# Kernel tuning notes

Measured on AMD Instinct MI355X. Metric: run time of the kernel, lower is better.

## Reference

```python
import jax, jax.numpy as jnp
import numpy as np

K = 10        # n_functions (random MLP draws)
H = 20        # hidden width of each tiny per-feature MLP
LN_EPS = 1e-5 # torch LayerNorm default eps
STD_EPS = 1e-8


def _layernorm(h):
    # LayerNorm over last dim, affine weight=1, bias=0 (torch default init),
    # biased variance, eps=1e-5.
    mu = h.mean(-1, keepdims=True)
    var = ((h - mu) ** 2).mean(-1, keepdims=True)
    return (h - mu) * jax.lax.rsqrt(var + LN_EPS)


def setup_inputs() -> dict:
    key = jax.random.key(0)
    B, T, N = 128, 256, 16
    ks = jax.random.split(key, 7)
    inputs = jax.random.normal(ks[0], (B, T, N), dtype=jnp.float32)

    def u(k, shape, bound):
        return jax.random.uniform(k, shape, minval=-bound, maxval=bound, dtype=jnp.float32)

    # torch Linear default init: uniform(-1/sqrt(fan_in), 1/sqrt(fan_in)) for W and b
    W1 = u(ks[1], (K, N, H), 1.0)        # Linear(1,20): fan_in=1
    b1 = u(ks[2], (K, N, H), 1.0)
    bnd = 1.0 / np.sqrt(H)
    W2 = u(ks[3], (K, N, H, H), bnd)     # Linear(20,20), weight layout [out,in]
    b2 = u(ks[4], (K, N, H), bnd)
    W3 = u(ks[5], (K, N, H), bnd)        # Linear(20,1) weight squeezed to [H]
    b3 = u(ks[6], (K, N), bnd)
    return {"inputs": inputs, "W1": W1, "b1": b1, "W2": W2, "b2": b2, "W3": W3, "b3": b3}


def reference(inputs, W1, b1, W2, b2, W3, b3):
    x = inputs.astype(jnp.float32)
    # standardize over batch dim (torch .std is unbiased, ddof=1)
    x = (x - x.mean(0)) / x.std(0, ddof=1)

    # All K draws x all N per-feature MLPs as one batched computation.
    # h: [K, B, T, N, H]
    h = jax.nn.relu(x[None, ..., None] * W1[:, None, None] + b1[:, None, None])
    h = _layernorm(h)
    h = jax.nn.relu(jnp.einsum('kbtni,knoi->kbtno', h, W2) + b2[:, None, None])
    h = _layernorm(h)
    t = jnp.einsum('kbtni,kni->kbtn', h, W3) + b3[:, None, None]   # [K, B, T, N]

    # std_out: standardize over batch dim
    t = (t - t.mean(1, keepdims=True)) / (t.std(1, ddof=1, keepdims=True) + STD_EPS)

    m_marginals = t.mean(1)                   # [K, T, N]
    prod_marginals = jnp.prod(m_marginals, -1)  # [K, T]
    prod_joint = jnp.prod(t, -1).mean(1)        # [K, T]
    per_k_mse = jnp.mean((prod_marginals - prod_joint) ** 2, axis=-1)  # [K]
    return jnp.mean(per_k_mse)
```

## Files before the change

### kernel.cpp

```cpp
#include <hip/hip_runtime.h>
#include <math.h>

#define B_ 128
#define T_ 256
#define N_ 16
#define K_ 10
#define H_ 20
#define TN_ (T_ * N_)
#define S_ (T_ * B_)

#define REP20(F) F(0) F(1) F(2) F(3) F(4) F(5) F(6) F(7) F(8) F(9) \
                 F(10) F(11) F(12) F(13) F(14) F(15) F(16) F(17) F(18) F(19)
#define REP16(F) F(0) F(1) F(2) F(3) F(4) F(5) F(6) F(7) F(8) F(9) \
                 F(10) F(11) F(12) F(13) F(14) F(15)

__device__ __forceinline__ float wsum(float v)
{
#pragma unroll
    for (int off = 32; off; off >>= 1) v += __shfl_xor(v, off);
    return v;
}

__global__ __launch_bounds__(256) void k_std(const float* __restrict__ x,
                                             float* __restrict__ xs2)
{
    const int wid = (blockIdx.x * 256 + threadIdx.x) >> 6;
    const int l   = threadIdx.x & 63;
    const int tt  = wid >> 4;
    const int n   = wid & 15;

    const float a0 = x[l * TN_ + wid];
    const float a1 = x[(64 + l) * TN_ + wid];

    const float sm = wsum(a0 + a1);
    const float mu = sm * (1.f / 128.f);

    const float d0 = a0 - mu, d1 = a1 - mu;
    const float vv = wsum(fmaf(d0, d0, d1 * d1));
    const float r  = __builtin_amdgcn_rsqf(vv * (1.f / 127.f));

    float* col = xs2 + ((size_t)n * T_ + tt) * B_;
    col[l]      = d0 * r;
    col[64 + l] = d1 * r;
}

__global__ __launch_bounds__(256) void k_mlp(
    const float* __restrict__ xs2,
    const float* __restrict__ W1, const float* __restrict__ b1,
    const float* __restrict__ W2, const float* __restrict__ b2,
    const float* __restrict__ W3, const float* __restrict__ b3,
    float* __restrict__ tb)
{
    const int kn = blockIdx.y;
    const int n  = kn & 15;

    const float* __restrict__ w1  = W1 + kn * H_;
    const float* __restrict__ bb1 = b1 + kn * H_;
    const float* __restrict__ w2  = W2 + kn * H_ * H_;
    const float* __restrict__ bb2 = b2 + kn * H_;
    const float* __restrict__ w3  = W3 + kn * H_;
    const float  bb3 = b3[kn];

    const int q = blockIdx.x * 256 + threadIdx.x;
    const float u = xs2[n * S_ + q];

#define DECLH(i) float h##i;
    REP20(DECLH)
    float s1 = 0.f;
#define L1(i) h##i = fmaxf(fmaf(u, w1[i], bb1[i]), 0.f); s1 += h##i;
    REP20(L1)
    const float mu1 = s1 * (1.f / H_);
    float v1 = 0.f;
#define VAR1(i) { const float d = h##i - mu1; v1 = fmaf(d, d, v1); }
    REP20(VAR1)
    const float r1  = __builtin_amdgcn_rsqf(v1 * (1.f / H_) + 1e-5f);
    const float mr1 = mu1 * r1;
#define NRM1(i) h##i = fmaf(h##i, r1, -mr1);
    REP20(NRM1)

#define DECLG(i) float g##i;
    REP20(DECLG)
    float s2 = 0.f;
#define L2I(o, i) acc = fmaf(h##i, w2[(o) * 20 + (i)], acc);
#define L2ROW(o) { float acc = bb2[o]; \
    L2I(o,0) L2I(o,1) L2I(o,2) L2I(o,3) L2I(o,4) \
    L2I(o,5) L2I(o,6) L2I(o,7) L2I(o,8) L2I(o,9) \
    L2I(o,10) L2I(o,11) L2I(o,12) L2I(o,13) L2I(o,14) \
    L2I(o,15) L2I(o,16) L2I(o,17) L2I(o,18) L2I(o,19) \
    g##o = fmaxf(acc, 0.f); s2 += g##o; }
    REP20(L2ROW)

    const float mu2 = s2 * (1.f / H_);
    float v2 = 0.f;
#define VAR2(o) { const float d = g##o - mu2; v2 = fmaf(d, d, v2); }
    REP20(VAR2)
    const float r2  = __builtin_amdgcn_rsqf(v2 * (1.f / H_) + 1e-5f);
    const float mr2 = mu2 * r2;

    float t = bb3;
#define L3(o) t = fmaf(fmaf(g##o, r2, -mr2), w3[o], t);
    REP20(L3)

    const int tt = q >> 7;
    const int b  = q & 127;
    tb[(((size_t)(kn >> 4) * T_ + tt) * N_ + n) * B_ + b] = t;
}

__global__ __launch_bounds__(256) void k_out(const float* __restrict__ tb,
                                             float* __restrict__ out)
{
    const int gw = (blockIdx.x * 256 + threadIdx.x) >> 6;
    const int l  = threadIdx.x & 63;
    const float* __restrict__ base = tb + (size_t)gw * (N_ * B_);

#define DECLZ(n) float z0_##n = base[(n) * B_ + l], z1_##n = base[(n) * B_ + 64 + l];
    REP16(DECLZ)

#define STDZ(n) { \
    const float sm = wsum(z0_##n + z1_##n); \
    const float mu = sm * (1.f / 128.f); \
    const float d0 = z0_##n - mu, d1 = z1_##n - mu; \
    const float vv = wsum(fmaf(d0, d0, d1 * d1)); \
    const float rr = 1.f / (sqrtf(vv * (1.f / 127.f)) + 1e-8f); \
    z0_##n = d0 * rr; z1_##n = d1 * rr; }
    REP16(STDZ)

    float p0 = 1.f, p1 = 1.f;
#define PRODZ(n) p0 *= z0_##n; p1 *= z1_##n;
    REP16(PRODZ)
    const float pj = wsum(p0 + p1) * (1.f / 128.f);

    if (l == 0)
        atomicAdd(out, pj * pj * (1.f / (K_ * T_)));
}

extern "C" void kernel_launch(void* const* d_in, const int* in_sizes, int n_in,
                              void* d_out, int out_size, void* d_ws, size_t ws_size,
                              hipStream_t stream)
{
    const float* x  = (const float*)d_in[0];
    const float* W1 = (const float*)d_in[1];
    const float* b1 = (const float*)d_in[2];
    const float* W2 = (const float*)d_in[3];
    const float* b2 = (const float*)d_in[4];
    const float* W3 = (const float*)d_in[5];
    const float* b3 = (const float*)d_in[6];
    float* out = (float*)d_out;

    char* ws = (char*)d_ws;
    float* xs2 = (float*)ws;
    float* tb  = (float*)(ws + (size_t)2 * 1024 * 1024);

    hipMemsetAsync(out, 0, sizeof(float), stream);

    k_std<<<(TN_ * 64) / 256, 256, 0, stream>>>(x, xs2);

    dim3 g2(S_ / 256, K_ * N_);
    k_mlp<<<g2, 256, 0, stream>>>(xs2, W1, b1, W2, b2, W3, b3, tb);

    k_out<<<(K_ * T_ * 64) / 256, 256, 0, stream>>>(tb, out);
}
```

Before: 199.4 us.

## Fuse standardization, per-feature MLP and output reduction into one kernel

Replaces the three-kernel pipeline with one kernel per (32 columns of T*N, k) block. The block stages inputs in shared memory, standardizes each column over the batch, runs the MLP with each lane handling two batch elements, standardizes outputs, and reduces the products in shared memory. This removes the global-memory round trips for the standardized inputs and the MLP outputs, plus two launches. In exchange, the batch standardization is recomputed for every k, the grid is only 1280 blocks, and register pressure is higher under a 3-waves-per-SIMD launch bound.

```diff
diff --git a/kernel.cpp b/kernel.cpp
--- a/kernel.cpp
+++ b/kernel.cpp
@@ -6,13 +6,11 @@
 #define N_ 16
 #define K_ 10
 #define H_ 20
-#define TN_ (T_ * N_)
-#define S_ (T_ * B_)
+#define TN_ 4096
+#define TQ_ 128
 
 #define REP20(F) F(0) F(1) F(2) F(3) F(4) F(5) F(6) F(7) F(8) F(9) \
                  F(10) F(11) F(12) F(13) F(14) F(15) F(16) F(17) F(18) F(19)
-#define REP16(F) F(0) F(1) F(2) F(3) F(4) F(5) F(6) F(7) F(8) F(9) \
-                 F(10) F(11) F(12) F(13) F(14) F(15)
 
 __device__ __forceinline__ float wsum(float v)
 {
@@ -21,117 +19,144 @@
     return v;
 }
 
-__global__ __launch_bounds__(256) void k_std(const float* __restrict__ x,
-                                             float* __restrict__ xs2)
-{
-    const int wid = (blockIdx.x * 256 + threadIdx.x) >> 6;
-    const int l   = threadIdx.x & 63;
-    const int tt  = wid >> 4;
-    const int n   = wid & 15;
-
-    const float a0 = x[l * TN_ + wid];
-    const float a1 = x[(64 + l) * TN_ + wid];
-
-    const float sm = wsum(a0 + a1);
-    const float mu = sm * (1.f / 128.f);
-
-    const float d0 = a0 - mu, d1 = a1 - mu;
-    const float vv = wsum(fmaf(d0, d0, d1 * d1));
-    const float r  = __builtin_amdgcn_rsqf(vv * (1.f / 127.f));
-
-    float* col = xs2 + ((size_t)n * T_ + tt) * B_;
-    col[l]      = d0 * r;
-    col[64 + l] = d1 * r;
-}
-
-__global__ __launch_bounds__(256) void k_mlp(
-    const float* __restrict__ xs2,
+__global__ __launch_bounds__(256, 3) void k_all(
+    const float* __restrict__ x,
     const float* __restrict__ W1, const float* __restrict__ b1,
     const float* __restrict__ W2, const float* __restrict__ b2,
     const float* __restrict__ W3, const float* __restrict__ b3,
-    float* __restrict__ tb)
+    float* __restrict__ out)
 {
-    const int kn = blockIdx.y;
-    const int n  = kn & 15;
+    __shared__ float xz[32 * 129];
+    __shared__ float zl[32 * 128];
+    __shared__ float pjp[4];
 
-    const float* __restrict__ w1  = W1 + kn * H_;
-    const float* __restrict__ bb1 = b1 + kn * H_;
-    const float* __restrict__ w2  = W2 + kn * H_ * H_;
-    const float* __restrict__ bb2 = b2 + kn * H_;
-    const float* __restrict__ w3  = W3 + kn * H_;
-    const float  bb3 = b3[kn];
+    const int tq  = blockIdx.x;
+    const int k   = blockIdx.y;
+    const int tid = threadIdx.x;
+    const int wv  = tid >> 6;
+    const int l   = tid & 63;
 
-    const int q = blockIdx.x * 256 + threadIdx.x;
-    const float u = xs2[n * S_ + q];
+#pragma unroll
+    for (int r = 0; r < 4; ++r) {
+        const int g4 = r * 1024 + tid * 4;
+        const int b  = g4 >> 5;
+        const int d0 = g4 & 31;
+        const float4 v = *reinterpret_cast<const float4*>(x + b * TN_ + tq * 32 + d0);
+        xz[(d0 + 0) * 129 + b] = v.x;
+        xz[(d0 + 1) * 129 + b] = v.y;
+        xz[(d0 + 2) * 129 + b] = v.z;
+        xz[(d0 + 3) * 129 + b] = v.w;
+    }
+    __syncthreads();
 
-#define DECLH(i) float h##i;
-    REP20(DECLH)
-    float s1 = 0.f;
-#define L1(i) h##i = fmaxf(fmaf(u, w1[i], bb1[i]), 0.f); s1 += h##i;
-    REP20(L1)
-    const float mu1 = s1 * (1.f / H_);
-    float v1 = 0.f;
-#define VAR1(i) { const float d = h##i - mu1; v1 = fmaf(d, d, v1); }
-    REP20(VAR1)
-    const float r1  = __builtin_amdgcn_rsqf(v1 * (1.f / H_) + 1e-5f);
-    const float mr1 = mu1 * r1;
-#define NRM1(i) h##i = fmaf(h##i, r1, -mr1);
-    REP20(NRM1)
+#pragma unroll
+    for (int c = 0; c < 8; ++c) {
+        const int col = wv * 8 + c;
+        const float a0 = xz[col * 129 + l];
+        const float a1 = xz[col * 129 + 64 + l];
+        const float mu = wsum(a0 + a1) * (1.f / 128.f);
+        const float d0 = a0 - mu, d1 = a1 - mu;
+        const float r  = __builtin_amdgcn_rsqf(wsum(fmaf(d0, d0, d1 * d1)) * (1.f / 127.f));
+        xz[col * 129 + l]      = d0 * r;
+        xz[col * 129 + 64 + l] = d1 * r;
+    }
+    __syncthreads();
 
-#define DECLG(i) float g##i;
-    REP20(DECLG)
-    float s2 = 0.f;
-#define L2I(o, i) acc = fmaf(h##i, w2[(o) * 20 + (i)], acc);
-#define L2ROW(o) { float acc = bb2[o]; \
-    L2I(o,0) L2I(o,1) L2I(o,2) L2I(o,3) L2I(o,4) \
-    L2I(o,5) L2I(o,6) L2I(o,7) L2I(o,8) L2I(o,9) \
-    L2I(o,10) L2I(o,11) L2I(o,12) L2I(o,13) L2I(o,14) \
-    L2I(o,15) L2I(o,16) L2I(o,17) L2I(o,18) L2I(o,19) \
-    g##o = fmaxf(acc, 0.f); s2 += g##o; }
-    REP20(L2ROW)
+#pragma unroll 1
+    for (int it = 0; it < 8; ++it) {
+        const int col = wv * 8 + it;
+        const int kn  = k * 16 + (col & 15);
 
-    const float mu2 = s2 * (1.f / H_);
-    float v2 = 0.f;
-#define VAR2(o) { const float d = g##o - mu2; v2 = fmaf(d, d, v2); }
-    REP20(VAR2)
-    const float r2  = __builtin_amdgcn_rsqf(v2 * (1.f / H_) + 1e-5f);
-    const float mr2 = mu2 * r2;
+        const float u0 = xz[col * 129 + l];
+        const float u1 = xz[col * 129 + 64 + l];
 
-    float t = bb3;
-#define L3(o) t = fmaf(fmaf(g##o, r2, -mr2), w3[o], t);
-    REP20(L3)
+        const float4* __restrict__ w1v = reinterpret_cast<const float4*>(W1 + kn * 20);
+        const float4* __restrict__ b1v = reinterpret_cast<const float4*>(b1 + kn * 20);
+        const float4* __restrict__ w2v = reinterpret_cast<const float4*>(W2 + kn * 400);
+        const float4* __restrict__ b2v = reinterpret_cast<const float4*>(b2 + kn * 20);
+        const float4* __restrict__ w3v = reinterpret_cast<const float4*>(W3 + kn * 20);
+        const float  bb3 = b3[kn];
 
-    const int tt = q >> 7;
-    const int b  = q & 127;
-    tb[(((size_t)(kn >> 4) * T_ + tt) * N_ + n) * B_ + b] = t;
-}
+#define DECLH(i) float ha##i, hb##i;
+        REP20(DECLH)
+        float s1a = 0.f, s1b = 0.f;
+#define L1C(c,i0,i1,i2,i3) { const float4 w = w1v[c]; const float4 bb = b1v[c]; \
+        ha##i0 = fmaxf(fmaf(u0, w.x, bb.x), 0.f); hb##i0 = fmaxf(fmaf(u1, w.x, bb.x), 0.f); s1a += ha##i0; s1b += hb##i0; \
+        ha##i1 = fmaxf(fmaf(u0, w.y, bb.y), 0.f); hb##i1 = fmaxf(fmaf(u1, w.y, bb.y), 0.f); s1a += ha##i1; s1b += hb##i1; \
+        ha##i2 = fmaxf(fmaf(u0, w.z, bb.z), 0.f); hb##i2 = fmaxf(fmaf(u1, w.z, bb.z), 0.f); s1a += ha##i2; s1b += hb##i2; \
+        ha##i3 = fmaxf(fmaf(u0, w.w, bb.w), 0.f); hb##i3 = fmaxf(fmaf(u1, w.w, bb.w), 0.f); s1a += ha##i3; s1b += hb##i3; }
+        L1C(0,0,1,2,3) L1C(1,4,5,6,7) L1C(2,8,9,10,11) L1C(3,12,13,14,15) L1C(4,16,17,18,19)
 
-__global__ __launch_bounds__(256) void k_out(const float* __restrict__ tb,
-                                             float* __restrict__ out)
-{
-    const int gw = (blockIdx.x * 256 + threadIdx.x) >> 6;
-    const int l  = threadIdx.x & 63;
-    const float* __restrict__ base = tb + (size_t)gw * (N_ * B_);
+        const float mu1a = s1a * 0.05f, mu1b = s1b * 0.05f;
+        float v1a = 0.f, v1b = 0.f;
+#define VAR1(i) { float d = ha##i - mu1a; v1a = fmaf(d, d, v1a); d = hb##i - mu1b; v1b = fmaf(d, d, v1b); }
+        REP20(VAR1)
+        const float r1a = __builtin_amdgcn_rsqf(v1a * 0.05f + 1e-5f);
+        const float r1b = __builtin_amdgcn_rsqf(v1b * 0.05f + 1e-5f);
+        const float m1a = mu1a * r1a, m1b = mu1b * r1b;
+#define NRM1(i) ha##i = fmaf(ha##i, r1a, -m1a); hb##i = fmaf(hb##i, r1b, -m1b);
+        REP20(NRM1)
 
-#define DECLZ(n) float z0_##n = base[(n) * B_ + l], z1_##n = base[(n) * B_ + 64 + l];
-    REP16(DECLZ)
+#define DECLG(i) float ga##i, gb##i;
+        REP20(DECLG)
+        float s2a = 0.f, s2b = 0.f;
+#define L2C(o,c,i0,i1,i2,i3) { const float4 w = w2v[(o) * 5 + (c)]; \
+        acca = fmaf(ha##i0, w.x, acca); acca = fmaf(ha##i1, w.y, acca); \
+        acca = fmaf(ha##i2, w.z, acca); acca = fmaf(ha##i3, w.w, acca); \
+        accb = fmaf(hb##i0, w.x, accb); accb = fmaf(hb##i1, w.y, accb); \
+        accb = fmaf(hb##i2, w.z, accb); accb = fmaf(hb##i3, w.w, accb); }
+#define L2ROW(o,bo) { float acca = (bo), accb = (bo); \
+        L2C(o,0,0,1,2,3) L2C(o,1,4,5,6,7) L2C(o,2,8,9,10,11) \
+        L2C(o,3,12,13,14,15) L2C(o,4,16,17,18,19) \
+        ga##o = fmaxf(acca, 0.f); s2a += ga##o; gb##o = fmaxf(accb, 0.f); s2b += gb##o; }
+        {
+            const float4 b2c0 = b2v[0], b2c1 = b2v[1], b2c2 = b2v[2], b2c3 = b2v[3], b2c4 = b2v[4];
+            L2ROW(0,  b2c0.x) L2ROW(1,  b2c0.y) L2ROW(2,  b2c0.z) L2ROW(3,  b2c0.w)
+            L2ROW(4,  b2c1.x) L2ROW(5,  b2c1.y) L2ROW(6,  b2c1.z) L2ROW(7,  b2c1.w)
+            L2ROW(8,  b2c2.x) L2ROW(9,  b2c2.y) L2ROW(10, b2c2.z) L2ROW(11, b2c2.w)
+            L2ROW(12, b2c3.x) L2ROW(13, b2c3.y) L2ROW(14, b2c3.z) L2ROW(15, b2c3.w)
+            L2ROW(16, b2c4.x) L2ROW(17, b2c4.y) L2ROW(18, b2c4.z) L2ROW(19, b2c4.w)
+        }
 
-#define STDZ(n) { \
-    const float sm = wsum(z0_##n + z1_##n); \
-    const float mu = sm * (1.f / 128.f); \
-    const float d0 = z0_##n - mu, d1 = z1_##n - mu; \
-    const float vv = wsum(fmaf(d0, d0, d1 * d1)); \
-    const float rr = 1.f / (sqrtf(vv * (1.f / 127.f)) + 1e-8f); \
-    z0_##n = d0 * rr; z1_##n = d1 * rr; }
-    REP16(STDZ)
+        const float mu2a = s2a * 0.05f, mu2b = s2b * 0.05f;
+        float v2a = 0.f, v2b = 0.f;
+#define VAR2(i) { float d = ga##i - mu2a; v2a = fmaf(d, d, v2a); d = gb##i - mu2b; v2b = fmaf(d, d, v2b); }
+        REP20(VAR2)
+        const float r2a = __builtin_amdgcn_rsqf(v2a * 0.05f + 1e-5f);
+        const float r2b = __builtin_amdgcn_rsqf(v2b * 0.05f + 1e-5f);
+        const float m2a = mu2a * r2a, m2b = mu2b * r2b;
 
-    float p0 = 1.f, p1 = 1.f;
-#define PRODZ(n) p0 *= z0_##n; p1 *= z1_##n;
-    REP16(PRODZ)
-    const float pj = wsum(p0 + p1) * (1.f / 128.f);
+        float t0 = bb3, t1 = bb3;
+#define L3C(c,i0,i1,i2,i3) { const float4 w = w3v[c]; \
+        t0 = fmaf(fmaf(ga##i0, r2a, -m2a), w.x, t0); t1 = fmaf(fmaf(gb##i0, r2b, -m2b), w.x, t1); \
+        t0 = fmaf(fmaf(ga##i1, r2a, -m2a), w.y, t0); t1 = fmaf(fmaf(gb##i1, r2b, -m2b), w.y, t1); \
+        t0 = fmaf(fmaf(ga##i2, r2a, -m2a), w.z, t0); t1 = fmaf(fmaf(gb##i2, r2b, -m2b), w.z, t1); \
+        t0 = fmaf(fmaf(ga##i3, r2a, -m2a), w.w, t0); t1 = fmaf(fmaf(gb##i3, r2b, -m2b), w.w, t1); }
+        L3C(0,0,1,2,3) L3C(1,4,5,6,7) L3C(2,8,9,10,11) L3C(3,12,13,14,15) L3C(4,16,17,18,19)
 
-    if (l == 0)
-        atomicAdd(out, pj * pj * (1.f / (K_ * T_)));
+        const float smu = wsum(t0 + t1) * (1.f / 128.f);
+        const float e0 = t0 - smu, e1 = t1 - smu;
+        const float sd = sqrtf(wsum(fmaf(e0, e0, e1 * e1)) * (1.f / 127.f));
+        const float rr = 1.f / (sd + 1e-8f);
+        zl[col * 128 + l]      = e0 * rr;
+        zl[col * 128 + 64 + l] = e1 * rr;
+    }
+    __syncthreads();
+
+    {
+        const int t_loc = wv >> 1;
+        const int b     = (wv & 1) * 64 + l;
+        float pj = zl[(t_loc * 16 + 0) * 128 + b];
+#pragma unroll
+        for (int n = 1; n < 16; ++n) pj *= zl[(t_loc * 16 + n) * 128 + b];
+        const float ps = wsum(pj);
+        if (l == 0) pjp[wv] = ps;
+    }
+    __syncthreads();
+    if (tid < 2) {
+        const float pjm = (pjp[tid * 2] + pjp[tid * 2 + 1]) * (1.f / 128.f);
+        atomicAdd(out, pjm * pjm * (1.f / (K_ * T_)));
+    }
 }
 
 extern "C" void kernel_launch(void* const* d_in, const int* in_sizes, int n_in,
@@ -147,16 +172,8 @@
     const float* b3 = (const float*)d_in[6];
     float* out = (float*)d_out;
 
-    char* ws = (char*)d_ws;
-    float* xs2 = (float*)ws;
-    float* tb  = (float*)(ws + (size_t)2 * 1024 * 1024);
-
     hipMemsetAsync(out, 0, sizeof(float), stream);
 
-    k_std<<<(TN_ * 64) / 256, 256, 0, stream>>>(x, xs2);
-
-    dim3 g2(S_ / 256, K_ * N_);
-    k_mlp<<<g2, 256, 0, stream>>>(xs2, W1, b1, W2, b2, W3, b3, tb);
-
-    k_out<<<(K_ * T_ * 64) / 256, 256, 0, stream>>>(tb, out);
+    dim3 grid(TQ_, K_);
+    k_all<<<grid, 256, 0, stream>>>(x, W1, b1, W2, b2, W3, b3, out);
 }
```

After: 236.4 us. 18.6% more time.

## Run hidden 20x20 layer on bf16 MFMA with hi/lo split and fused LN epilogue

Applied to the files above, without the earlier changes.

The per-thread scalar 20x20 FMA layer is replaced by MFMA 16x16x32 bf16 matrix ops. Activations and weights are staged in shared memory and split into hi/lo bf16 parts, using three MFMAs to approximate fp32 accuracy. The second LayerNorm and the W3 projection are folded into a one-pass sum/sumsq/dot reduction across lanes. The final atomicAdd is replaced by per-row partials plus a double-precision reduction kernel, and the memset is removed. This adds LDS traffic and shuffles, and drops the lo*lo term, which lowers precision slightly.

```diff
diff --git a/kernel.cpp b/kernel.cpp
--- a/kernel.cpp
+++ b/kernel.cpp
@@ -6,8 +6,13 @@
 #define N_ 16
 #define K_ 10
 #define H_ 20
-#define TN_ (T_ * N_)
-#define S_ (T_ * B_)
+#define TN_ 4096
+#define S_ 32768
+
+typedef __attribute__((ext_vector_type(8))) short bf16x8;
+typedef __attribute__((ext_vector_type(4))) float f32x4;
+
+union U4B { uint4 u; bf16x8 b; };
 
 #define REP20(F) F(0) F(1) F(2) F(3) F(4) F(5) F(6) F(7) F(8) F(9) \
                  F(10) F(11) F(12) F(13) F(14) F(15) F(16) F(17) F(18) F(19)
@@ -21,6 +26,15 @@
     return v;
 }
 
+__device__ __forceinline__ void split2(float a, float b, unsigned& hi, unsigned& lo)
+{
+    const unsigned au = __float_as_uint(a), bu = __float_as_uint(b);
+    hi = (au >> 16) | (bu & 0xffff0000u);
+    const float ra = a - __uint_as_float(au & 0xffff0000u);
+    const float rb = b - __uint_as_float(bu & 0xffff0000u);
+    lo = (__float_as_uint(ra) >> 16) | (__float_as_uint(rb) & 0xffff0000u);
+}
+
 __global__ __launch_bounds__(256) void k_std(const float* __restrict__ x,
                                              float* __restrict__ xs2)
 {
@@ -32,12 +46,9 @@
     const float a0 = x[l * TN_ + wid];
     const float a1 = x[(64 + l) * TN_ + wid];
 
-    const float sm = wsum(a0 + a1);
-    const float mu = sm * (1.f / 128.f);
-
+    const float mu = wsum(a0 + a1) * (1.f / 128.f);
     const float d0 = a0 - mu, d1 = a1 - mu;
-    const float vv = wsum(fmaf(d0, d0, d1 * d1));
-    const float r  = __builtin_amdgcn_rsqf(vv * (1.f / 127.f));
+    const float r  = __builtin_amdgcn_rsqf(wsum(fmaf(d0, d0, d1 * d1)) * (1.f / 127.f));
 
     float* col = xs2 + ((size_t)n * T_ + tt) * B_;
     col[l]      = d0 * r;
@@ -51,87 +62,177 @@
     const float* __restrict__ W3, const float* __restrict__ b3,
     float* __restrict__ tb)
 {
-    const int kn = blockIdx.y;
-    const int n  = kn & 15;
-
-    const float* __restrict__ w1  = W1 + kn * H_;
-    const float* __restrict__ bb1 = b1 + kn * H_;
-    const float* __restrict__ w2  = W2 + kn * H_ * H_;
-    const float* __restrict__ bb2 = b2 + kn * H_;
-    const float* __restrict__ w3  = W3 + kn * H_;
+    __shared__ unsigned hs[256 * 28];
+    __shared__ unsigned wB[32 * 28];
+    __shared__ float sb2[32], sw3[32];
+
+    const int kn  = blockIdx.y;
+    const int k   = kn >> 4;
+    const int n   = kn & 15;
+    const int tid = threadIdx.x;
+    const int w   = tid >> 6;
+    const int L   = tid & 63;
+    const int g   = L >> 4;
+    const int r16 = L & 15;
+    const int q0b = blockIdx.x * 256;
+
+    const float* __restrict__ w2c = W2 + kn * 400;
+    for (int j = tid; j < 320; j += 256) {
+        const int o = j / 10, kp = j % 10;
+        unsigned hi = 0u, lo = 0u;
+        if (o < 20)
+            split2(w2c[o * 20 + 2 * kp], w2c[o * 20 + 2 * kp + 1], hi, lo);
+        wB[o * 28 + kp]      = hi;
+        wB[o * 28 + 12 + kp] = lo;
+    }
+    if (tid < 128) {
+        const int o = tid >> 2, c = tid & 3;
+        wB[o * 28 + ((c < 2) ? 10 + c : 20 + c)] = 0u;
+    }
+    if (tid < 32) {
+        sb2[tid] = (tid < 20) ? b2[kn * 20 + tid] : 0.f;
+        sw3[tid] = (tid < 20) ? W3[kn * 20 + tid] : 0.f;
+    }
+
+    const float* __restrict__ w1c = W1 + kn * H_;
+    const float* __restrict__ b1c = b1 + kn * H_;
+    const float* __restrict__ w3c = W3 + kn * H_;
     const float  bb3 = b3[kn];
-
-    const int q = blockIdx.x * 256 + threadIdx.x;
-    const float u = xs2[n * S_ + q];
-
+    float w3sum = 0.f;
+#define W3S(i) w3sum += w3c[i];
+    REP20(W3S)
+
+    const float u = xs2[n * S_ + q0b + tid];
 #define DECLH(i) float h##i;
     REP20(DECLH)
     float s1 = 0.f;
-#define L1(i) h##i = fmaxf(fmaf(u, w1[i], bb1[i]), 0.f); s1 += h##i;
+#define L1(i) h##i = fmaxf(fmaf(u, w1c[i], b1c[i]), 0.f); s1 += h##i;
     REP20(L1)
-    const float mu1 = s1 * (1.f / H_);
+    const float mu1 = s1 * 0.05f;
     float v1 = 0.f;
 #define VAR1(i) { const float d = h##i - mu1; v1 = fmaf(d, d, v1); }
     REP20(VAR1)
-    const float r1  = __builtin_amdgcn_rsqf(v1 * (1.f / H_) + 1e-5f);
-    const float mr1 = mu1 * r1;
-#define NRM1(i) h##i = fmaf(h##i, r1, -mr1);
+    const float r1 = __builtin_amdgcn_rsqf(v1 * 0.05f + 1e-5f);
+    const float m1 = mu1 * r1;
+#define NRM1(i) h##i = fmaf(h##i, r1, -m1);
     REP20(NRM1)
 
-#define DECLG(i) float g##i;
-    REP20(DECLG)
-    float s2 = 0.f;
-#define L2I(o, i) acc = fmaf(h##i, w2[(o) * 20 + (i)], acc);
-#define L2ROW(o) { float acc = bb2[o]; \
-    L2I(o,0) L2I(o,1) L2I(o,2) L2I(o,3) L2I(o,4) \
-    L2I(o,5) L2I(o,6) L2I(o,7) L2I(o,8) L2I(o,9) \
-    L2I(o,10) L2I(o,11) L2I(o,12) L2I(o,13) L2I(o,14) \
-    L2I(o,15) L2I(o,16) L2I(o,17) L2I(o,18) L2I(o,19) \
-    g##o = fmaxf(acc, 0.f); s2 += g##o; }
-    REP20(L2ROW)
-
-    const float mu2 = s2 * (1.f / H_);
-    float v2 = 0.f;
-#define VAR2(o) { const float d = g##o - mu2; v2 = fmaf(d, d, v2); }
-    REP20(VAR2)
-    const float r2  = __builtin_amdgcn_rsqf(v2 * (1.f / H_) + 1e-5f);
-    const float mr2 = mu2 * r2;
-
-    float t = bb3;
-#define L3(o) t = fmaf(fmaf(g##o, r2, -mr2), w3[o], t);
-    REP20(L3)
-
-    const int tt = q >> 7;
-    const int b  = q & 127;
-    tb[(((size_t)(kn >> 4) * T_ + tt) * N_ + n) * B_ + b] = t;
-}
-
-__global__ __launch_bounds__(256) void k_out(const float* __restrict__ tb,
-                                             float* __restrict__ out)
-{
-    const int gw = (blockIdx.x * 256 + threadIdx.x) >> 6;
+    {
+        unsigned* row = hs + tid * 28;
+        unsigned hi, lo;
+#define PKW(m, i0, i1) split2(h##i0, h##i1, hi, lo); row[m] = hi; row[12 + m] = lo;
+        PKW(0, 0, 1) PKW(1, 2, 3) PKW(2, 4, 5) PKW(3, 6, 7) PKW(4, 8, 9)
+        PKW(5, 10, 11) PKW(6, 12, 13) PKW(7, 14, 15) PKW(8, 16, 17) PKW(9, 18, 19)
+        *reinterpret_cast<uint2*>(row + 10) = make_uint2(0u, 0u);
+        *reinterpret_cast<uint2*>(row + 22) = make_uint2(0u, 0u);
+    }
+    __syncthreads();
+
+    const int slhi = (g < 2) ? g * 4 : 8;
+    const int sllo = 12 + slhi;
+    U4B bh0, bl0, bh1, bl1;
+    bh0.u = *reinterpret_cast<const uint4*>(wB + r16 * 28 + slhi);
+    bl0.u = *reinterpret_cast<const uint4*>(wB + r16 * 28 + sllo);
+    bh1.u = *reinterpret_cast<const uint4*>(wB + (16 + r16) * 28 + slhi);
+    bl1.u = *reinterpret_cast<const uint4*>(wB + (16 + r16) * 28 + sllo);
+    const float b2_0 = sb2[r16],      b2_1 = sb2[16 + r16];
+    const float w3_0 = sw3[r16],      w3_1 = sw3[16 + r16];
+    const unsigned keepA = (g < 3) ? 0xffffffffu : 0u;
+    const unsigned keepB = (g < 2) ? 0xffffffffu : 0u;
+
+#pragma unroll
+    for (int p = 0; p < 4; ++p) {
+        const int rowA = w * 64 + p * 16 + r16;
+        U4B ah, al;
+        ah.u = *reinterpret_cast<const uint4*>(hs + rowA * 28 + slhi);
+        al.u = *reinterpret_cast<const uint4*>(hs + rowA * 28 + sllo);
+        ah.u.x &= keepA; ah.u.y &= keepA; ah.u.z &= keepB; ah.u.w &= keepB;
+        al.u.x &= keepA; al.u.y &= keepA; al.u.z &= keepB; al.u.w &= keepB;
+
+        f32x4 a0 = {0.f, 0.f, 0.f, 0.f}, a1 = {0.f, 0.f, 0.f, 0.f};
+        a0 = __builtin_amdgcn_mfma_f32_16x16x32_bf16(ah.b, bl0.b, a0, 0, 0, 0);
+        a0 = __builtin_amdgcn_mfma_f32_16x16x32_bf16(al.b, bh0.b, a0, 0, 0, 0);
+        a0 = __builtin_amdgcn_mfma_f32_16x16x32_bf16(ah.b, bh0.b, a0, 0, 0, 0);
+        a1 = __builtin_amdgcn_mfma_f32_16x16x32_bf16(ah.b, bl1.b, a1, 0, 0, 0);
+        a1 = __builtin_amdgcn_mfma_f32_16x16x32_bf16(al.b, bh1.b, a1, 0, 0, 0);
+        a1 = __builtin_amdgcn_mfma_f32_16x16x32_bf16(ah.b, bh1.b, a1, 0, 0, 0);
+
+#define EPI(r) \
+        const float g0_##r = fmaxf(a0[r] + b2_0, 0.f); \
+        const float g1_##r = fmaxf(a1[r] + b2_1, 0.f); \
+        float S1_##r = g0_##r + g1_##r; \
+        float S2_##r = fmaf(g0_##r, g0_##r, g1_##r * g1_##r); \
+        float S3_##r = fmaf(g0_##r, w3_0, g1_##r * w3_1);
+        EPI(0) EPI(1) EPI(2) EPI(3)
+#undef EPI
+
+#define R16X(v) { v += __shfl_xor(v, 1); v += __shfl_xor(v, 2); \
+                  v += __shfl_xor(v, 4); v += __shfl_xor(v, 8); }
+        R16X(S1_0) R16X(S1_1) R16X(S1_2) R16X(S1_3)
+        R16X(S2_0) R16X(S2_1) R16X(S2_2) R16X(S2_3)
+        R16X(S3_0) R16X(S3_1) R16X(S3_2) R16X(S3_3)
+#undef R16X
+
+#define TFIN(r) \
+        const float mu_##r  = S1_##r * 0.05f; \
+        const float var_##r = fmaf(-mu_##r, mu_##r, S2_##r * 0.05f); \
+        const float rq_##r  = __builtin_amdgcn_rsqf(var_##r + 1e-5f); \
+        const float t_##r   = fmaf(rq_##r, S3_##r, fmaf(-mu_##r * rq_##r, w3sum, bb3));
+        TFIN(0) TFIN(1) TFIN(2) TFIN(3)
+#undef TFIN
+
+        if (r16 < 4) {
+            const float ts = (r16 == 0) ? t_0 : (r16 == 1) ? t_1
+                           : (r16 == 2) ? t_2 : t_3;
+            const int q = q0b + w * 64 + p * 16 + g * 4 + r16;
+            tb[(((size_t)k * T_ + (q >> 7)) * N_ + n) * B_ + (q & 127)] = ts;
+        }
+    }
+}
+
+__global__ __launch_bounds__(256) void k_fin(const float* __restrict__ tb,
+                                             float* __restrict__ partials)
+{
+    const int gw = blockIdx.x * 4 + (threadIdx.x >> 6);
     const int l  = threadIdx.x & 63;
     const float* __restrict__ base = tb + (size_t)gw * (N_ * B_);
 
 #define DECLZ(n) float z0_##n = base[(n) * B_ + l], z1_##n = base[(n) * B_ + 64 + l];
     REP16(DECLZ)
+#undef DECLZ
 
 #define STDZ(n) { \
-    const float sm = wsum(z0_##n + z1_##n); \
-    const float mu = sm * (1.f / 128.f); \
+    const float mu = wsum(z0_##n + z1_##n) * (1.f / 128.f); \
     const float d0 = z0_##n - mu, d1 = z1_##n - mu; \
     const float vv = wsum(fmaf(d0, d0, d1 * d1)); \
     const float rr = 1.f / (sqrtf(vv * (1.f / 127.f)) + 1e-8f); \
     z0_##n = d0 * rr; z1_##n = d1 * rr; }
     REP16(STDZ)
+#undef STDZ
 
     float p0 = 1.f, p1 = 1.f;
 #define PRODZ(n) p0 *= z0_##n; p1 *= z1_##n;
     REP16(PRODZ)
+#undef PRODZ
     const float pj = wsum(p0 + p1) * (1.f / 128.f);
 
     if (l == 0)
-        atomicAdd(out, pj * pj * (1.f / (K_ * T_)));
+        partials[gw] = pj * pj * (1.f / (K_ * T_));
+}
+
+__global__ __launch_bounds__(256) void k_sum(const float* __restrict__ partials,
+                                             float* __restrict__ out)
+{
+    __shared__ double sred[4];
+    const int tid = threadIdx.x;
+    double a = 0.0;
+#pragma unroll
+    for (int j = 0; j < 10; ++j) a += (double)partials[j * 256 + tid];
+#pragma unroll
+    for (int off = 32; off; off >>= 1) a += __shfl_xor(a, off);
+    if ((tid & 63) == 0) sred[tid >> 6] = a;
+    __syncthreads();
+    if (tid == 0) out[0] = (float)(sred[0] + sred[1] + sred[2] + sred[3]);
 }
 
 extern "C" void kernel_launch(void* const* d_in, const int* in_sizes, int n_in,
@@ -148,15 +249,15 @@
     float* out = (float*)d_out;
 
     char* ws = (char*)d_ws;
-    float* xs2 = (float*)ws;
-    float* tb  = (float*)(ws + (size_t)2 * 1024 * 1024);
-
-    hipMemsetAsync(out, 0, sizeof(float), stream);
-
-    k_std<<<(TN_ * 64) / 256, 256, 0, stream>>>(x, xs2);
+    float* xs2      = (float*)ws;
+    float* tb       = (float*)(ws + 2097152);
+    float* partials = (float*)(ws + 23068672);
+
+    k_std<<<1024, 256, 0, stream>>>(x, xs2);
 
     dim3 g2(S_ / 256, K_ * N_);
     k_mlp<<<g2, 256, 0, stream>>>(xs2, W1, b1, W2, b2, W3, b3, tb);
 
-    k_out<<<(K_ * T_ * 64) / 256, 256, 0, stream>>>(tb, out);
-}
+    k_fin<<<(K_ * T_) / 4, 256, 0, stream>>>(tb, partials);
+    k_sum<<<1, 256, 0, stream>>>(partials, out);
+}
```

New measurement: 273.9 us. 1.37x slower.
